# Kernel optimization log

Measured on AMD Instinct MI355X. Metric: run time of the kernel, lower is better.

The kernel has to match this reference:

```python
import jax, jax.numpy as jnp
import numpy as np

HALF_LOG_2PI = 0.5 * float(np.log(2.0 * np.pi))


def setup_inputs() -> dict:
    key = jax.random.key(0)
    k1, k2 = jax.random.split(key)
    N, D = 16384, 2048
    x = jax.random.normal(k1, (N, D), dtype=jnp.float32)
    raw_params = jax.random.normal(k2, (2 * D,), dtype=jnp.float32)
    # chain spanning tree: edges (i, i+1) for i in 0..D-2  -> shape [D-1, 2]
    idx = jnp.arange(D - 1, dtype=jnp.int64)
    edges = jnp.stack([idx, idx + 1], axis=1)
    return {"x": x, "raw_params": raw_params, "edges": edges}


def reference(x, raw_params, edges):
    # x: [N, D] float; raw_params: [2D] float; edges: [E, 2] int
    D = x.shape[1]
    means = jnp.tanh(raw_params[:D]) * 2.0               # [D]
    stds = jax.nn.softplus(raw_params[D:]) + 1e-6         # [D]
    # Each edge (i, j) contributes logN(x_i) + logN(x_j); equivalently each
    # feature k contributes deg(k) * logN(x_k), deg = endpoint multiplicity.
    deg = jnp.zeros((D,), dtype=x.dtype).at[edges.reshape(-1)].add(1.0)  # [D]
    z = (x - means) / stds                                # [N, D]
    logp = -0.5 * z * z - jnp.log(stds) - HALF_LOG_2PI    # [N, D]
    return logp @ deg                                     # [N]
```

## Files before the change

### kernel.cpp

```cpp
#include <hip/hip_runtime.h>
#include <math.h>

#define HALF_LOG_2PI_F 0.9189385332046727f

__global__ void clt_prep_kernel(const float* __restrict__ rp,
                                const int* __restrict__ edges,
                                float* __restrict__ A,
                                float* __restrict__ B,
                                float* __restrict__ csum,
                                int D, int E) {
    extern __shared__ float sdeg[];
    for (int k = threadIdx.x; k < D; k += blockDim.x) sdeg[k] = 0.0f;
    __syncthreads();
    for (int e = threadIdx.x; e < E; e += blockDim.x) {
        int i = edges[2 * e];
        int j = edges[2 * e + 1];
        atomicAdd(&sdeg[i], 1.0f);
        atomicAdd(&sdeg[j], 1.0f);
    }
    __syncthreads();

    float local_c = 0.0f;
    for (int k = threadIdx.x; k < D; k += blockDim.x) {
        float m = tanhf(rp[k]) * 2.0f;
        float sx = rp[D + k];
        float s = fmaxf(sx, 0.0f) + log1pf(expf(-fabsf(sx))) + 1e-6f;
        float inv_s2 = 1.0f / (s * s);
        float deg = sdeg[k];
        A[k] = deg * (-0.5f * inv_s2);
        B[k] = deg * (m * inv_s2);
        local_c += deg * (-0.5f * m * m * inv_s2 - logf(s) - HALF_LOG_2PI_F);
    }

    __shared__ float wsum[16];
    for (int off = 32; off > 0; off >>= 1)
        local_c += __shfl_down(local_c, off, 64);
    int wid = threadIdx.x >> 6;
    int lane = threadIdx.x & 63;
    if (lane == 0) wsum[wid] = local_c;
    __syncthreads();
    if (threadIdx.x == 0) {
        float t = 0.0f;
        int nw = (blockDim.x + 63) >> 6;
        for (int w = 0; w < nw; ++w) t += wsum[w];
        *csum = t;
    }
}

template <int NI>
__global__ __launch_bounds__(256) void clt_rows_fast(
        const float* __restrict__ x,
        const float* __restrict__ A,
        const float* __restrict__ B,
        const float* __restrict__ csum,
        float* __restrict__ out,
        int D, int N, int total_waves) {
    const int lane = threadIdx.x & 63;
    const int gwave = blockIdx.x * (blockDim.x >> 6) + (threadIdx.x >> 6);

    const float4* Av = (const float4*)A;
    const float4* Bv = (const float4*)B;
    float4 a4[NI], b4[NI];
#pragma unroll
    for (int i = 0; i < NI; ++i) {
        a4[i] = Av[i * 64 + lane];
        b4[i] = Bv[i * 64 + lane];
    }
    const float c = *csum;

    for (int r = gwave; r < N; r += total_waves) {
        const float4* xv = (const float4*)(x + (size_t)r * (size_t)D);
        float acc0 = 0.0f, acc1 = 0.0f;
#pragma unroll
        for (int i = 0; i < NI; ++i) {
            float4 xq = xv[i * 64 + lane];
            acc0 += xq.x * fmaf(a4[i].x, xq.x, b4[i].x);
            acc1 += xq.y * fmaf(a4[i].y, xq.y, b4[i].y);
            acc0 += xq.z * fmaf(a4[i].z, xq.z, b4[i].z);
            acc1 += xq.w * fmaf(a4[i].w, xq.w, b4[i].w);
        }
        float acc = acc0 + acc1;
#pragma unroll
        for (int off = 32; off > 0; off >>= 1)
            acc += __shfl_down(acc, off, 64);
        if (lane == 0) out[r] = acc + c;
    }
}

__global__ __launch_bounds__(256) void clt_row_generic(
        const float* __restrict__ x,
        const float* __restrict__ A,
        const float* __restrict__ B,
        const float* __restrict__ csum,
        float* __restrict__ out,
        int D) {
    const int row = blockIdx.x;
    float acc = 0.0f;
    for (int k = threadIdx.x; k < D; k += blockDim.x) {
        float xs = x[(size_t)row * (size_t)D + k];
        acc += xs * fmaf(A[k], xs, B[k]);
    }
    for (int off = 32; off > 0; off >>= 1)
        acc += __shfl_down(acc, off, 64);
    __shared__ float wsum[4];
    int wid = threadIdx.x >> 6;
    int lane = threadIdx.x & 63;
    if (lane == 0) wsum[wid] = acc;
    __syncthreads();
    if (threadIdx.x == 0)
        out[row] = wsum[0] + wsum[1] + wsum[2] + wsum[3] + *csum;
}

extern "C" void kernel_launch(void* const* d_in, const int* in_sizes, int n_in,
                              void* d_out, int out_size, void* d_ws, size_t ws_size,
                              hipStream_t stream) {
    const float* x     = (const float*)d_in[0];
    const float* rp    = (const float*)d_in[1];
    const int*   edges = (const int*)d_in[2];
    float* out = (float*)d_out;

    const int D = in_sizes[1] / 2;
    const int E = in_sizes[2] / 2;
    const int N = out_size;

    float* A    = (float*)d_ws;
    float* B    = A + D;
    float* csum = B + D;

    clt_prep_kernel<<<1, 1024, D * sizeof(float), stream>>>(rp, edges, A, B, csum, D, E);

    const int NI = D / 256;
    if (D % 256 == 0 && (NI == 2 || NI == 4 || NI == 8 || NI == 16)) {
        int waves = (N + 3) / 4;
        int blocks = (waves + 3) / 4;
        if (blocks < 64) blocks = 64;
        if (blocks > 4096) blocks = 4096;
        int total_waves = blocks * 4;
        switch (NI) {
            case 2:  clt_rows_fast<2><<<blocks, 256, 0, stream>>>(x, A, B, csum, out, D, N, total_waves); break;
            case 4:  clt_rows_fast<4><<<blocks, 256, 0, stream>>>(x, A, B, csum, out, D, N, total_waves); break;
            case 8:  clt_rows_fast<8><<<blocks, 256, 0, stream>>>(x, A, B, csum, out, D, N, total_waves); break;
            default: clt_rows_fast<16><<<blocks, 256, 0, stream>>>(x, A, B, csum, out, D, N, total_waves); break;
        }
    } else {
        clt_row_generic<<<N, 256, 0, stream>>>(x, A, B, csum, out, D);
    }
}
```

Baseline: 35.60 us.

## Fuse parameter prep into row kernel with per-block LDS coefficients and row pairing

Removes the separate single-block prep launch. Each block of the row kernel now rebuilds the degree histogram, A/B coefficients and the constant term in LDS itself, then streams x. Each wave processes two rows per iteration using nontemporal vector loads, and the grid is fixed at 512 blocks. This trades redundant per-block prep work (edge atomics and transcendentals) for eliminating a serialized launch and the global round-trip of A, B and the constant.

```diff
diff --git a/kernel.cpp b/kernel.cpp
--- a/kernel.cpp
+++ b/kernel.cpp
@@ -2,6 +2,91 @@
 #include <math.h>
 
 #define HALF_LOG_2PI_F 0.9189385332046727f
+
+typedef float f32x4 __attribute__((ext_vector_type(4)));
+
+template <int NI>
+__global__ __launch_bounds__(256) void clt_fused(
+        const float* __restrict__ x,
+        const float* __restrict__ rp,
+        const int* __restrict__ edges,
+        float* __restrict__ out,
+        int D, int E, int N, int total_waves) {
+    extern __shared__ __align__(16) float smem[];
+    float* sdeg = smem;
+    float* As   = smem + D;
+    float* Bs   = smem + 2 * D;
+
+    const int tid = threadIdx.x;
+
+    for (int k = tid; k < D; k += 256) sdeg[k] = 0.0f;
+    __syncthreads();
+    for (int e = tid; e < E; e += 256) {
+        atomicAdd(&sdeg[edges[2 * e]], 1.0f);
+        atomicAdd(&sdeg[edges[2 * e + 1]], 1.0f);
+    }
+    __syncthreads();
+
+    float local_c = 0.0f;
+    for (int k = tid; k < D; k += 256) {
+        float m = tanhf(rp[k]) * 2.0f;
+        float sx = rp[D + k];
+        float s = fmaxf(sx, 0.0f) + log1pf(expf(-fabsf(sx))) + 1e-6f;
+        float inv_s2 = 1.0f / (s * s);
+        float deg = sdeg[k];
+        As[k] = deg * (-0.5f * inv_s2);
+        Bs[k] = deg * (m * inv_s2);
+        local_c += deg * (-0.5f * m * m * inv_s2 - logf(s) - HALF_LOG_2PI_F);
+    }
+#pragma unroll
+    for (int off = 32; off > 0; off >>= 1)
+        local_c += __shfl_down(local_c, off, 64);
+    __shared__ float wsum[4];
+    if ((tid & 63) == 0) wsum[tid >> 6] = local_c;
+    __syncthreads();
+    const float c = wsum[0] + wsum[1] + wsum[2] + wsum[3];
+
+    const int lane = tid & 63;
+    const f32x4* Av = (const f32x4*)As;
+    const f32x4* Bv = (const f32x4*)Bs;
+    f32x4 a4[NI], b4[NI];
+#pragma unroll
+    for (int i = 0; i < NI; ++i) {
+        a4[i] = Av[i * 64 + lane];
+        b4[i] = Bv[i * 64 + lane];
+    }
+
+    const int gwave = blockIdx.x * 4 + (tid >> 6);
+    for (int r = gwave * 2; r < N; r += total_waves * 2) {
+        const f32x4* xv0 = (const f32x4*)(x + (size_t)r * (size_t)D);
+        const f32x4* xv1 = (const f32x4*)(x + (size_t)(r + 1) * (size_t)D);
+        float p0 = 0.0f, q0 = 0.0f, p1 = 0.0f, q1 = 0.0f;
+#pragma unroll
+        for (int i = 0; i < NI; ++i) {
+            f32x4 x0 = __builtin_nontemporal_load(&xv0[i * 64 + lane]);
+            f32x4 x1 = __builtin_nontemporal_load(&xv1[i * 64 + lane]);
+            p0 += x0.x * fmaf(a4[i].x, x0.x, b4[i].x);
+            q0 += x0.y * fmaf(a4[i].y, x0.y, b4[i].y);
+            p0 += x0.z * fmaf(a4[i].z, x0.z, b4[i].z);
+            q0 += x0.w * fmaf(a4[i].w, x0.w, b4[i].w);
+            p1 += x1.x * fmaf(a4[i].x, x1.x, b4[i].x);
+            q1 += x1.y * fmaf(a4[i].y, x1.y, b4[i].y);
+            p1 += x1.z * fmaf(a4[i].z, x1.z, b4[i].z);
+            q1 += x1.w * fmaf(a4[i].w, x1.w, b4[i].w);
+        }
+        float acc0 = p0 + q0;
+        float acc1 = p1 + q1;
+#pragma unroll
+        for (int off = 32; off > 0; off >>= 1) {
+            acc0 += __shfl_down(acc0, off, 64);
+            acc1 += __shfl_down(acc1, off, 64);
+        }
+        if (lane == 0) {
+            out[r] = acc0 + c;
+            out[r + 1] = acc1 + c;
+        }
+    }
+}
 
 __global__ void clt_prep_kernel(const float* __restrict__ rp,
                                 const int* __restrict__ edges,
@@ -13,13 +98,10 @@
     for (int k = threadIdx.x; k < D; k += blockDim.x) sdeg[k] = 0.0f;
     __syncthreads();
     for (int e = threadIdx.x; e < E; e += blockDim.x) {
-        int i = edges[2 * e];
-        int j = edges[2 * e + 1];
-        atomicAdd(&sdeg[i], 1.0f);
-        atomicAdd(&sdeg[j], 1.0f);
+        atomicAdd(&sdeg[edges[2 * e]], 1.0f);
+        atomicAdd(&sdeg[edges[2 * e + 1]], 1.0f);
     }
     __syncthreads();
-
     float local_c = 0.0f;
     for (int k = threadIdx.x; k < D; k += blockDim.x) {
         float m = tanhf(rp[k]) * 2.0f;
@@ -31,59 +113,16 @@
         B[k] = deg * (m * inv_s2);
         local_c += deg * (-0.5f * m * m * inv_s2 - logf(s) - HALF_LOG_2PI_F);
     }
-
     __shared__ float wsum[16];
     for (int off = 32; off > 0; off >>= 1)
         local_c += __shfl_down(local_c, off, 64);
-    int wid = threadIdx.x >> 6;
-    int lane = threadIdx.x & 63;
-    if (lane == 0) wsum[wid] = local_c;
+    if ((threadIdx.x & 63) == 0) wsum[threadIdx.x >> 6] = local_c;
     __syncthreads();
     if (threadIdx.x == 0) {
         float t = 0.0f;
         int nw = (blockDim.x + 63) >> 6;
         for (int w = 0; w < nw; ++w) t += wsum[w];
         *csum = t;
-    }
-}
-
-template <int NI>
-__global__ __launch_bounds__(256) void clt_rows_fast(
-        const float* __restrict__ x,
-        const float* __restrict__ A,
-        const float* __restrict__ B,
-        const float* __restrict__ csum,
-        float* __restrict__ out,
-        int D, int N, int total_waves) {
-    const int lane = threadIdx.x & 63;
-    const int gwave = blockIdx.x * (blockDim.x >> 6) + (threadIdx.x >> 6);
-
-    const float4* Av = (const float4*)A;
-    const float4* Bv = (const float4*)B;
-    float4 a4[NI], b4[NI];
-#pragma unroll
-    for (int i = 0; i < NI; ++i) {
-        a4[i] = Av[i * 64 + lane];
-        b4[i] = Bv[i * 64 + lane];
-    }
-    const float c = *csum;
-
-    for (int r = gwave; r < N; r += total_waves) {
-        const float4* xv = (const float4*)(x + (size_t)r * (size_t)D);
-        float acc0 = 0.0f, acc1 = 0.0f;
-#pragma unroll
-        for (int i = 0; i < NI; ++i) {
-            float4 xq = xv[i * 64 + lane];
-            acc0 += xq.x * fmaf(a4[i].x, xq.x, b4[i].x);
-            acc1 += xq.y * fmaf(a4[i].y, xq.y, b4[i].y);
-            acc0 += xq.z * fmaf(a4[i].z, xq.z, b4[i].z);
-            acc1 += xq.w * fmaf(a4[i].w, xq.w, b4[i].w);
-        }
-        float acc = acc0 + acc1;
-#pragma unroll
-        for (int off = 32; off > 0; off >>= 1)
-            acc += __shfl_down(acc, off, 64);
-        if (lane == 0) out[r] = acc + c;
     }
 }
 
@@ -103,9 +142,7 @@
     for (int off = 32; off > 0; off >>= 1)
         acc += __shfl_down(acc, off, 64);
     __shared__ float wsum[4];
-    int wid = threadIdx.x >> 6;
-    int lane = threadIdx.x & 63;
-    if (lane == 0) wsum[wid] = acc;
+    if ((threadIdx.x & 63) == 0) wsum[threadIdx.x >> 6] = acc;
     __syncthreads();
     if (threadIdx.x == 0)
         out[row] = wsum[0] + wsum[1] + wsum[2] + wsum[3] + *csum;
@@ -123,26 +160,24 @@
     const int E = in_sizes[2] / 2;
     const int N = out_size;
 
-    float* A    = (float*)d_ws;
-    float* B    = A + D;
-    float* csum = B + D;
-
-    clt_prep_kernel<<<1, 1024, D * sizeof(float), stream>>>(rp, edges, A, B, csum, D, E);
-
     const int NI = D / 256;
-    if (D % 256 == 0 && (NI == 2 || NI == 4 || NI == 8 || NI == 16)) {
-        int waves = (N + 3) / 4;
-        int blocks = (waves + 3) / 4;
-        if (blocks < 64) blocks = 64;
-        if (blocks > 4096) blocks = 4096;
-        int total_waves = blocks * 4;
+    const bool fast = (D % 256 == 0) && (N % 2 == 0) &&
+                      (NI == 2 || NI == 4 || NI == 8 || NI == 16);
+    if (fast) {
+        const int blocks = 512;
+        const int total_waves = blocks * 4;
+        const size_t lds = (size_t)3 * D * sizeof(float);
         switch (NI) {
-            case 2:  clt_rows_fast<2><<<blocks, 256, 0, stream>>>(x, A, B, csum, out, D, N, total_waves); break;
-            case 4:  clt_rows_fast<4><<<blocks, 256, 0, stream>>>(x, A, B, csum, out, D, N, total_waves); break;
-            case 8:  clt_rows_fast<8><<<blocks, 256, 0, stream>>>(x, A, B, csum, out, D, N, total_waves); break;
-            default: clt_rows_fast<16><<<blocks, 256, 0, stream>>>(x, A, B, csum, out, D, N, total_waves); break;
+            case 2:  clt_fused<2><<<blocks, 256, lds, stream>>>(x, rp, edges, out, D, E, N, total_waves); break;
+            case 4:  clt_fused<4><<<blocks, 256, lds, stream>>>(x, rp, edges, out, D, E, N, total_waves); break;
+            case 8:  clt_fused<8><<<blocks, 256, lds, stream>>>(x, rp, edges, out, D, E, N, total_waves); break;
+            default: clt_fused<16><<<blocks, 256, lds, stream>>>(x, rp, edges, out, D, E, N, total_waves); break;
         }
     } else {
+        float* A    = (float*)d_ws;
+        float* B    = A + D;
+        float* csum = B + D;
+        clt_prep_kernel<<<1, 1024, D * sizeof(float), stream>>>(rp, edges, A, B, csum, D, E);
         clt_row_generic<<<N, 256, 0, stream>>>(x, A, B, csum, out, D);
     }
 }
```

Measured after the change: 39.44 us. +10.8%, slower.
